# Performance work log

Measured on AMD Instinct MI355X. Metric: run time of the kernel, lower is better.

## Reference

```python
import jax, jax.numpy as jnp
import numpy as np

NHEADS = 16
SCALE_BASE = 512
GN_EPS = 1e-5


def rotate_every_two(x):
    x1 = x[..., ::2]
    x2 = x[..., 1::2]
    return jnp.stack((-x2, x1), axis=-1).reshape(x.shape)


def xpos_apply(x, downscale, offset=0):
    # x: [B, T, C]; XPOS over the FULL embedding dim (applied before head split)
    B, T, C = x.shape
    half = C // 2
    scale_vec = (jnp.arange(0, C, 2, dtype=jnp.float32) + 0.4 * C) / (1.4 * C)  # [half]
    min_pos = -(T + offset) // 2
    max_pos = T + offset + min_pos
    power = jnp.arange(min_pos, max_pos, dtype=jnp.float32) / SCALE_BASE  # [L]
    scale = scale_vec[None, :] ** power[:, None]  # [L, half]
    L = scale.shape[0]
    inv_freq = 1.0 / (10000.0 ** (jnp.arange(half, dtype=jnp.float32) / half))
    sinusoid = jnp.arange(L, dtype=jnp.float32)[:, None] * inv_freq[None, :]  # [L, half]
    sin, cos = jnp.sin(sinusoid), jnp.cos(sinusoid)
    if L > T:
        scale, sin, cos = scale[-T:], sin[-T:], cos[-T:]
    if downscale:
        scale = 1.0 / scale
    sin = jnp.repeat(sin * scale, 2, axis=-1)  # [T, C] (duplicate_interleave)
    cos = jnp.repeat(cos * scale, 2, axis=-1)
    return x * cos + rotate_every_two(x) * sin


def decay_mask(nheads, T):
    gamma = 1.0 - 2.0 ** (-5.0 - jnp.arange(nheads, dtype=jnp.float32))  # [H]
    idx = jnp.arange(T)
    diff = idx[:, None] - idx[None, :]  # [T, T]
    keep = diff >= 0
    m = gamma[:, None, None] ** jnp.where(keep, diff, 0).astype(jnp.float32)
    return jnp.where(keep[None, :, :], m, 0.0)  # [H, T, T]


def setup_inputs() -> dict:
    key = jax.random.key(0)
    ks = jax.random.split(key, 6)
    B, T, C = 2, 2048, 1024
    w_std = 0.02
    return {
        "x": jax.random.normal(ks[0], (B, T, C), jnp.float32),
        "w_qkvff": jax.random.normal(ks[1], (5 * C, C), jnp.float32) * w_std,
        "w_gated": jax.random.normal(ks[2], (C, C), jnp.float32) * w_std,
        "b_gated": jnp.zeros((C,), jnp.float32),
        "w_proj": jax.random.normal(ks[3], (C, C), jnp.float32) * w_std,
        "b_proj": jnp.zeros((C,), jnp.float32),
        "gn_w": jnp.ones((C,), jnp.float32),
        "gn_b": jnp.zeros((C,), jnp.float32),
        "w_ff": jax.random.normal(ks[4], (C, 2 * C), jnp.float32) * w_std,
        "rms_w": jnp.ones((C,), jnp.float32),
    }


def reference(x, w_qkvff, w_gated, b_gated, w_proj, b_proj, gn_w, gn_b, w_ff, rms_w):
    B, T, C = x.shape
    H = NHEADS
    hd = C // H
    # RMSNorm: x / clamp(||x|| * C^-0.5, 1e-8) * w
    nrm = jnp.sqrt(jnp.sum(x * x, axis=-1, keepdims=True)) * (C ** -0.5)
    x_ = x / jnp.maximum(nrm, 1e-8) * rms_w
    # fused qkvff projection (Linear, no bias): [B,T,5C]
    qkvff = jnp.einsum('btc,oc->bto', x_, w_qkvff)
    q, k, v, ff = jnp.split(qkvff, [C, 2 * C, 3 * C], axis=-1)
    q = xpos_apply(q, downscale=False)
    k = xpos_apply(k, downscale=True)
    # split heads -> [B,H,T,hd]
    q = q.reshape(B, T, H, hd).transpose(0, 2, 1, 3)
    k = k.reshape(B, T, H, hd).transpose(0, 2, 1, 3)
    v = v.reshape(B, T, H, hd).transpose(0, 2, 1, 3)
    # parallel retention: decay-masked QK^T @ V
    scores = jnp.einsum('bhtd,bhsd->bhts', q, k) * (hd ** -0.5)
    scores = scores * decay_mask(H, T)[None]
    y = jnp.einsum('bhts,bhsd->bhtd', scores, v)  # [B,H,T,hd]
    # GroupNorm(H groups) applied over flattened (B*T, C)
    yg = y.transpose(0, 2, 1, 3).reshape(B * T, H, hd)
    mu = jnp.mean(yg, axis=-1, keepdims=True)
    var = jnp.mean((yg - mu) ** 2, axis=-1, keepdims=True)
    yg = (yg - mu) / jnp.sqrt(var + GN_EPS)
    y = yg.reshape(B * T, C) * gn_w + gn_b
    y = y.reshape(B, T, C)
    # gated SiLU on raw x (pre-norm), then output proj
    y = jax.nn.silu(jnp.einsum('btc,oc->bto', x, w_gated) + b_gated) * y
    y = jnp.einsum('btc,oc->bto', y, w_proj) + b_proj
    # gated FFN branch: exact (erf) GELU then Linear(2C->C, no bias)
    ff_out = jnp.einsum('bte,ce->btc', jax.nn.gelu(ff, approximate=False), w_ff)
    return x + ff_out + y
```

## Files before the change

kernel.cpp:

```cpp
#include <hip/hip_runtime.h>
#include <math.h>

#define B_  2
#define T_  2048
#define C_  1024
#define H_  16
#define FC_ 5120

typedef __attribute__((ext_vector_type(8))) short  s16x8;
typedef __attribute__((ext_vector_type(4))) float  f32x4;
typedef __attribute__((ext_vector_type(2))) unsigned short u16x2;
typedef __attribute__((ext_vector_type(4))) unsigned short u16x4;
typedef __attribute__((ext_vector_type(8))) unsigned short u16x8;

__device__ __forceinline__ ushort f2bf(float f) {
    union { float f; unsigned u; } v; v.f = f;
    unsigned r = v.u + 0x7FFFu + ((v.u >> 16) & 1u);
    return (ushort)(r >> 16);
}
__device__ __forceinline__ float bf2f(ushort u) {
    union { unsigned u; float f; } v; v.u = (unsigned)u << 16; return v.f;
}

__global__ __launch_bounds__(256) void cvt_bf16_kernel(const float* __restrict__ src,
                                                       ushort* __restrict__ dst, int n8) {
    int i = blockIdx.x * 256 + threadIdx.x;
    if (i >= n8) return;
    float4 a = ((const float4*)src)[2*i];
    float4 b = ((const float4*)src)[2*i + 1];
    u16x8 o;
    o[0] = f2bf(a.x); o[1] = f2bf(a.y); o[2] = f2bf(a.z); o[3] = f2bf(a.w);
    o[4] = f2bf(b.x); o[5] = f2bf(b.y); o[6] = f2bf(b.z); o[7] = f2bf(b.w);
    *(u16x8*)(dst + 8*i) = o;
}

__global__ __launch_bounds__(256) void rmsnorm_kernel(const float* __restrict__ x,
                                                      const float* __restrict__ rms_w,
                                                      ushort* __restrict__ xn) {
    int row = blockIdx.x;
    int tid = threadIdx.x;
    float4 v = ((const float4*)(x + (size_t)row * C_))[tid];
    float ss = v.x*v.x + v.y*v.y + v.z*v.z + v.w*v.w;
    #pragma unroll
    for (int m = 32; m >= 1; m >>= 1) ss += __shfl_xor(ss, m);
    __shared__ float wsum[4];
    if ((tid & 63) == 0) wsum[tid >> 6] = ss;
    __syncthreads();
    float tot = wsum[0] + wsum[1] + wsum[2] + wsum[3];
    float nrm = sqrtf(tot) * 0.03125f;
    float inv = 1.0f / fmaxf(nrm, 1e-8f);
    float4 w = ((const float4*)rms_w)[tid];
    u16x4 o;
    o[0] = f2bf(v.x * inv * w.x);  o[1] = f2bf(v.y * inv * w.y);
    o[2] = f2bf(v.z * inv * w.z);  o[3] = f2bf(v.w * inv * w.w);
    *(u16x4*)(xn + (size_t)row * C_ + 4*tid) = o;
}

__global__ __launch_bounds__(256) void xpos_bf16_kernel(const ushort* __restrict__ qktmp,
                                                        ushort* __restrict__ qkv) {
    int bt = blockIdx.x;
    int t = bt & (T_ - 1);
    float tf = (float)t;
    const ushort* row = qktmp + (size_t)bt * 2048;
    ushort* orow = qkv + (size_t)bt * 3072;
    float power = (tf - 1024.0f) * (1.0f / 512.0f);
    for (int i = threadIdx.x; i < 512; i += 256) {
        float sv    = (2.0f * (float)i + 409.6f) * (1.0f / 1433.6f);
        float scale = exp2f(power * log2f(sv));
        float invf  = exp2f((float)i * (-13.287712379549449f / 512.0f));
        float ang   = tf * invf;
        float sn, cs;
        sincosf(ang, &sn, &cs);
        float rs = 1.0f / scale;
        int hh = i >> 5;
        float lg2g = log2f(1.0f - exp2f(-5.0f - (float)hh));
        float gq = exp2f(lg2g * tf) * 0.125f;
        float gk = exp2f(-lg2g * tf);
        u16x2 qi = *(const u16x2*)(row + 2*i);
        u16x2 ki = *(const u16x2*)(row + 1024 + 2*i);
        float qx = bf2f(qi[0]), qy = bf2f(qi[1]);
        float kx = bf2f(ki[0]), ky = bf2f(ki[1]);
        float qox = (qx*(cs*scale) - qy*(sn*scale)) * gq;
        float qoy = (qy*(cs*scale) + qx*(sn*scale)) * gq;
        float kox = (kx*(cs*rs) - ky*(sn*rs)) * gk;
        float koy = (ky*(cs*rs) + kx*(sn*rs)) * gk;
        u16x2 qo; qo[0] = f2bf(qox); qo[1] = f2bf(qoy);
        u16x2 ko; ko[0] = f2bf(kox); ko[1] = f2bf(koy);
        *(u16x2*)(orow + 2*i) = qo;
        *(u16x2*)(orow + 1024 + 2*i) = ko;
    }
}

template<int EPI, int BN>
__global__ __launch_bounds__(256) void gemm_bf16_kernel(
        const ushort* __restrict__ A, int lda,
        const ushort* __restrict__ W, int ldw,
        float* __restrict__ Cmat, int ldc, int K,
        const float* __restrict__ bias,
        const float* __restrict__ add1,
        const float* __restrict__ add2,
        ushort* __restrict__ oqk,
        ushort* __restrict__ ov,
        ushort* __restrict__ offb) {
    constexpr int NG = BN / 32;
    __shared__ __align__(16) ushort As[128*64];
    __shared__ __align__(16) ushort Bs[BN*64];
    int tid = threadIdx.x;
    int m0 = blockIdx.y * 128, n0 = blockIdx.x * BN;
    int wave = tid >> 6, lane = tid & 63;
    int lo = lane & 15, hi = lane >> 4;
    int wm = (wave >> 1) * 64, wn = (wave & 1) * (BN/2);
    int sra = tid >> 3, sua = tid & 7;
    f32x4 acc[4][NG] = {};

    u16x8 ra[4], rb[4];
    auto loadA = [&](int k0) {
        #pragma unroll
        for (int i = 0; i < 4; ++i)
            ra[i] = *(const u16x8*)(A + (size_t)(m0 + sra + 32*i) * lda + k0 + sua*8);
    };
    auto loadB = [&](int k0) {
        if constexpr (BN == 128) {
            #pragma unroll
            for (int i = 0; i < 4; ++i)
                rb[i] = *(const u16x8*)(W + (size_t)(n0 + sra + 32*i) * ldw + k0 + sua*8);
        } else {
            int r = tid >> 2, c = tid & 3;
            rb[0] = *(const u16x8*)(W + (size_t)(n0 + r) * ldw + k0 + c*8);
            rb[1] = *(const u16x8*)(W + (size_t)(n0 + r) * ldw + k0 + (c+4)*8);
        }
    };
    loadA(0); loadB(0);
    for (int k0 = 0;;) {
        __syncthreads();
        #pragma unroll
        for (int i = 0; i < 4; ++i) {
            int row = sra + 32*i;
            *(u16x8*)((char*)As + (row*128 + ((sua*16) ^ ((row & 7) << 4)))) = ra[i];
        }
        if constexpr (BN == 128) {
            #pragma unroll
            for (int i = 0; i < 4; ++i) {
                int row = sra + 32*i;
                *(u16x8*)((char*)Bs + (row*128 + ((sua*16) ^ ((row & 7) << 4)))) = rb[i];
            }
        } else {
            int r = tid >> 2, c = tid & 3, sw = (r & 7) << 4;
            *(u16x8*)((char*)Bs + (r*128 + ((c*16) ^ sw)))     = rb[0];
            *(u16x8*)((char*)Bs + (r*128 + (((c+4)*16) ^ sw))) = rb[1];
        }
        __syncthreads();
        k0 += 64;
        if (k0 < K) { loadA(k0); loadB(k0); }
        #pragma unroll
        for (int kc = 0; kc < 2; ++kc) {
            s16x8 af[4], bf[NG];
            #pragma unroll
            for (int g = 0; g < 4; ++g) {
                int arow = wm + g*16 + lo;
                af[g] = *(const s16x8*)((const char*)As +
                         arow*128 + ((kc*64 + hi*16) ^ ((arow & 7) << 4)));
            }
            #pragma unroll
            for (int g = 0; g < NG; ++g) {
                int brow = wn + g*16 + lo;
                bf[g] = *(const s16x8*)((const char*)Bs +
                         brow*128 + ((kc*64 + hi*16) ^ ((brow & 7) << 4)));
            }
            #pragma unroll
            for (int mg = 0; mg < 4; ++mg)
                #pragma unroll
                for (int ng = 0; ng < NG; ++ng)
                    acc[mg][ng] = __builtin_amdgcn_mfma_f32_16x16x32_bf16(
                        af[mg], bf[ng], acc[mg][ng], 0, 0, 0);
        }
        if (k0 >= K) break;
    }
    #pragma unroll
    for (int mg = 0; mg < 4; ++mg) {
        #pragma unroll
        for (int r = 0; r < 4; ++r) {
            size_t m = (size_t)(m0 + wm + mg*16 + hi*4 + r);
            #pragma unroll
            for (int ng = 0; ng < NG; ++ng) {
                int n = n0 + wn + ng*16 + lo;
                float v = acc[mg][ng][r];
                if constexpr (EPI == 3) {
                    if (n0 < 2048)      oqk[m*2048 + n] = f2bf(v);
                    else if (n0 < 3072) ov[m*3072 + n] = f2bf(v);
                    else offb[m*2048 + (n - 3072)] =
                             f2bf(0.5f * v * (1.0f + erff(v * 0.70710678118f)));
                } else {
                    if (EPI == 1) {
                        float s = v + bias[n];
                        v = s / (1.0f + expf(-s));
                    } else if (EPI == 2) {
                        v += bias[n] + add1[m*ldc + n] + add2[m*ldc + n];
                    }
                    Cmat[m*ldc + n] = v;
                }
            }
        }
    }
}

__global__ __launch_bounds__(256) void attn_mfma2_kernel(const ushort* __restrict__ qkv,
                                                         float* __restrict__ y) {
    __shared__ ushort Ks[2][64*64];
    __shared__ ushort Vt[2][64*64];
    __shared__ ushort Ss[4][16*64];
    int F = blockIdx.x;
    int o = (F & 7) * 64 + (F >> 3);
    int tta = o & 15;
    int h   = (o >> 4) & 15;
    int b   = o >> 8;
    int ttb = 31 - tta;
    int t0a = tta * 64, t0b = ttb * 64;
    int tid = threadIdx.x;
    int wave = tid >> 6, lane = tid & 63;
    int lo = lane & 15, hi = lane >> 4;
    const size_t bT = (size_t)b * T_;

    const ushort* qra = qkv + (bT + t0a + wave*16 + lo) * 3072 + h*64;
    const ushort* qrb = qkv + (bT + t0b + wave*16 + lo) * 3072 + h*64;
    s16x8 qa0 = *(const s16x8*)(qra + hi*8);
    s16x8 qa1 = *(const s16x8*)(qra + 32 + hi*8);
    s16x8 qb0 = *(const s16x8*)(qrb + hi*8);
    s16x8 qb1 = *(const s16x8*)(qrb + 32 + hi*8);
    f32x4 acca[4] = {}, accb[4] = {};

    int kr = tid >> 2, kc = tid & 3;
    int vd0 = (tid & 15) * 4, vs0 = (tid >> 4) * 4;
    u16x8 rka, rkb;
    u16x4 rv0, rv1, rv2, rv3;
    auto loadt = [&](int s0) {
        const ushort* src = qkv + (bT + s0 + kr) * 3072 + 1024 + h*64;
        rka = *(const u16x8*)(src + kc*8);
        rkb = *(const u16x8*)(src + (kc+4)*8);
        const ushort* vsrc = qkv + (bT + s0 + vs0) * 3072 + 2048 + h*64 + vd0;
        rv0 = *(const u16x4*)(vsrc);
        rv1 = *(const u16x4*)(vsrc + 3072);
        rv2 = *(const u16x4*)(vsrc + 2*3072);
        rv3 = *(const u16x4*)(vsrc + 3*3072);
    };
    int cur = 0;
    loadt(0);
    for (int st = 0; st <= ttb; ++st) {
        {
            int base = kr * 128, sw = (kr & 7) << 4;
            *(u16x8*)((char*)Ks[cur] + ((base + kc*16) ^ sw))     = rka;
            *(u16x8*)((char*)Ks[cur] + ((base + (kc+4)*16) ^ sw)) = rkb;
            #pragma unroll
            for (int i = 0; i < 4; ++i) {
                u16x4 o4; o4[0] = rv0[i]; o4[1] = rv1[i]; o4[2] = rv2[i]; o4[3] = rv3[i];
                int d = vd0 + i;
                *(u16x4*)((char*)Vt[cur] + ((d*128 + vs0*2) ^ ((d & 7) << 4))) = o4;
            }
        }
        __syncthreads();
        if (st < ttb) loadt((st + 1) * 64);

        auto compute = [&](s16x8 q0, s16x8 q1, f32x4* accy, bool diag) {
            f32x4 sacc[4] = {};
            #pragma unroll
            for (int sn = 0; sn < 4; ++sn) {
                int srow = sn*16 + lo;
                int rb2 = srow * 128, sw = (srow & 7) << 4;
                s16x8 kf0 = *(const s16x8*)((const char*)Ks[cur] + ((rb2 + hi*16) ^ sw));
                s16x8 kf1 = *(const s16x8*)((const char*)Ks[cur] + ((rb2 + 64 + hi*16) ^ sw));
                sacc[sn] = __builtin_amdgcn_mfma_f32_16x16x32_bf16(q0, kf0, sacc[sn], 0, 0, 0);
                sacc[sn] = __builtin_amdgcn_mfma_f32_16x16x32_bf16(q1, kf1, sacc[sn], 0, 0, 0);
            }
            #pragma unroll
            for (int sn = 0; sn < 4; ++sn) {
                int sl = sn*16 + lo;
                #pragma unroll
                for (int r = 0; r < 4; ++r) {
                    float v = sacc[sn][r];
                    if (diag && sl > wave*16 + hi*4 + r) v = 0.0f;
                    int tq = hi*4 + r;
                    *(ushort*)((char*)Ss[wave] + ((tq*128 + sl*2) ^ ((tq & 7) << 4))) = f2bf(v);
                }
            }
            s16x8 sa0 = *(const s16x8*)((const char*)Ss[wave] + ((lo*128 + hi*16) ^ ((lo & 7) << 4)));
            s16x8 sa1 = *(const s16x8*)((const char*)Ss[wave] + ((lo*128 + 64 + hi*16) ^ ((lo & 7) << 4)));
            #pragma unroll
            for (int dn = 0; dn < 4; ++dn) {
                int d = dn*16 + lo;
                int rb2 = d * 128, sw = (d & 7) << 4;
                s16x8 vf0 = *(const s16x8*)((const char*)Vt[cur] + ((rb2 + hi*16) ^ sw));
                s16x8 vf1 = *(const s16x8*)((const char*)Vt[cur] + ((rb2 + 64 + hi*16) ^ sw));
                accy[dn] = __builtin_amdgcn_mfma_f32_16x16x32_bf16(sa0, vf0, accy[dn], 0, 0, 0);
                accy[dn] = __builtin_amdgcn_mfma_f32_16x16x32_bf16(sa1, vf1, accy[dn], 0, 0, 0);
            }
        };
        compute(qb0, qb1, accb, st == ttb);
        if (st <= tta) compute(qa0, qa1, acca, st == tta);
        cur ^= 1;
    }
    #pragma unroll
    for (int dn = 0; dn < 4; ++dn) {
        #pragma unroll
        for (int r = 0; r < 4; ++r) {
            int ta = t0a + wave*16 + hi*4 + r;
            int tb = t0b + wave*16 + hi*4 + r;
            y[(bT + ta) * C_ + h*64 + dn*16 + lo] = acca[dn][r];
            y[(bT + tb) * C_ + h*64 + dn*16 + lo] = accb[dn][r];
        }
    }
}

__global__ __launch_bounds__(256) void gn_gate_kernel(const float* __restrict__ y,
                                                      const float* __restrict__ gate,
                                                      const float* __restrict__ gn_w,
                                                      const float* __restrict__ gn_b,
                                                      ushort* __restrict__ ygb) {
    int bt = blockIdx.x;
    int tid = threadIdx.x;
    float4 v = ((const float4*)(y + (size_t)bt * C_))[tid];
    float s1 = v.x + v.y + v.z + v.w;
    float s2 = v.x*v.x + v.y*v.y + v.z*v.z + v.w*v.w;
    #pragma unroll
    for (int m = 1; m < 16; m <<= 1) { s1 += __shfl_xor(s1, m); s2 += __shfl_xor(s2, m); }
    float mu   = s1 * (1.0f/64.0f);
    float var  = s2 * (1.0f/64.0f) - mu*mu;
    float rstd = rsqrtf(var + 1e-5f);
    float4 w  = ((const float4*)gn_w)[tid];
    float4 bb = ((const float4*)gn_b)[tid];
    float4 g  = ((const float4*)(gate + (size_t)bt * C_))[tid];
    u16x4 o;
    o[0] = f2bf(((v.x - mu)*rstd*w.x + bb.x) * g.x);
    o[1] = f2bf(((v.y - mu)*rstd*w.y + bb.y) * g.y);
    o[2] = f2bf(((v.z - mu)*rstd*w.z + bb.z) * g.z);
    o[3] = f2bf(((v.w - mu)*rstd*w.w + bb.w) * g.w);
    *(u16x4*)(ygb + (size_t)bt * C_ + 4*tid) = o;
}

extern "C" void kernel_launch(void* const* d_in, const int* in_sizes, int n_in,
                              void* d_out, int out_size, void* d_ws, size_t ws_size,
                              hipStream_t stream) {
    (void)in_sizes; (void)n_in; (void)out_size; (void)ws_size;
    const float* x       = (const float*)d_in[0];
    const float* w_qkvff = (const float*)d_in[1];
    const float* w_gated = (const float*)d_in[2];
    const float* b_gated = (const float*)d_in[3];
    const float* w_proj  = (const float*)d_in[4];
    const float* b_proj  = (const float*)d_in[5];
    const float* gn_w    = (const float*)d_in[6];
    const float* gn_b    = (const float*)d_in[7];
    const float* w_ff    = (const float*)d_in[8];
    const float* rms_w   = (const float*)d_in[9];
    float* out = (float*)d_out;

    const size_t NTOK = (size_t)B_ * T_;
    float* buf0   = (float*)d_ws;
    float* buf1   = buf0 + NTOK * C_;
    float* buf2   = buf1 + NTOK * C_;
    ushort* qkvb  = (ushort*)(buf2 + NTOK * C_);
    ushort* qktmp = qkvb + NTOK * 3072;
    ushort* xb    = qktmp + NTOK * 2048;
    ushort* xnb   = xb + NTOK * C_;
    ushort* ffb   = xnb + NTOK * C_;
    ushort* ygb   = ffb + NTOK * 2048;
    ushort* wqb   = ygb + NTOK * C_;
    ushort* wgb   = wqb + (size_t)FC_ * C_;
    ushort* wpb   = wgb + (size_t)C_ * C_;
    ushort* wfb   = wpb + (size_t)C_ * C_;

    cvt_bf16_kernel<<<2048, 256, 0, stream>>>(x, xb, 524288);
    cvt_bf16_kernel<<<2560, 256, 0, stream>>>(w_qkvff, wqb, 655360);
    cvt_bf16_kernel<<<512,  256, 0, stream>>>(w_gated, wgb, 131072);
    cvt_bf16_kernel<<<512,  256, 0, stream>>>(w_proj,  wpb, 131072);
    cvt_bf16_kernel<<<1024, 256, 0, stream>>>(w_ff,    wfb, 262144);
    rmsnorm_kernel<<<4096, 256, 0, stream>>>(x, rms_w, xnb);
    gemm_bf16_kernel<3,128><<<dim3(40, 32), 256, 0, stream>>>(
        xnb, C_, wqb, C_, nullptr, 0, C_, nullptr, nullptr, nullptr, qktmp, qkvb, ffb);
    xpos_bf16_kernel<<<4096, 256, 0, stream>>>(qktmp, qkvb);
    attn_mfma2_kernel<<<512, 256, 0, stream>>>(qkvb, buf1);
    gemm_bf16_kernel<1,64><<<dim3(16, 32), 256, 0, stream>>>(
        xb, C_, wgb, C_, buf2, C_, C_, b_gated, nullptr, nullptr, nullptr, nullptr, nullptr);
    gn_gate_kernel<<<4096, 256, 0, stream>>>(buf1, buf2, gn_w, gn_b, ygb);
    gemm_bf16_kernel<0,64><<<dim3(16, 32), 256, 0, stream>>>(
        ffb, 2*C_, wfb, 2*C_, buf0, C_, 2*C_, nullptr, nullptr, nullptr, nullptr, nullptr, nullptr);
    gemm_bf16_kernel<2,64><<<dim3(16, 32), 256, 0, stream>>>(
        ygb, C_, wpb, C_, out, C_, C_, b_proj, x, buf0, nullptr, nullptr, nullptr);
}
```

Baseline: 324.4 us.

## Use direct global-to-LDS loads in GEMM and merge bf16 conversion launches

The GEMM tile loads now use global_load_lds to copy A and B tiles straight into shared memory. The XOR swizzle moves into the global column index, so the register staging and software prefetch of the next tile are gone. The five fp32-to-bf16 conversion launches are also merged into one kernel that picks its source by block index. In exchange, the GEMM loses its overlap of the next tile's loads with the current MFMA work, since loads are now issued after the barrier with no double buffering.

```diff
diff --git a/kernel.cpp b/kernel.cpp
--- a/kernel.cpp
+++ b/kernel.cpp
@@ -13,6 +13,9 @@
 typedef __attribute__((ext_vector_type(4))) unsigned short u16x4;
 typedef __attribute__((ext_vector_type(8))) unsigned short u16x8;
 
+#define AS1 __attribute__((address_space(1)))
+#define AS3 __attribute__((address_space(3)))
+
 __device__ __forceinline__ ushort f2bf(float f) {
     union { float f; unsigned u; } v; v.f = f;
     unsigned r = v.u + 0x7FFFu + ((v.u >> 16) & 1u);
@@ -21,17 +24,30 @@
 __device__ __forceinline__ float bf2f(ushort u) {
     union { unsigned u; float f; } v; v.u = (unsigned)u << 16; return v.f;
 }
-
-__global__ __launch_bounds__(256) void cvt_bf16_kernel(const float* __restrict__ src,
-                                                       ushort* __restrict__ dst, int n8) {
+__device__ __forceinline__ void gload16(const void* g, void* l) {
+    __builtin_amdgcn_global_load_lds((const AS1 unsigned int*)g,
+                                     (AS3 unsigned int*)l, 16, 0, 0);
+}
+
+__global__ __launch_bounds__(256) void cvt_all_kernel(
+        const float* __restrict__ x, const float* __restrict__ wq,
+        const float* __restrict__ wg, const float* __restrict__ wp,
+        const float* __restrict__ wf,
+        ushort* __restrict__ xb, ushort* __restrict__ wqb, ushort* __restrict__ wgb,
+        ushort* __restrict__ wpb, ushort* __restrict__ wfb) {
     int i = blockIdx.x * 256 + threadIdx.x;
-    if (i >= n8) return;
-    float4 a = ((const float4*)src)[2*i];
-    float4 b = ((const float4*)src)[2*i + 1];
+    const float* src; ushort* dst; int off;
+    if (i < 524288)       { src = x;  dst = xb;  off = i; }
+    else if (i < 1179648) { src = wq; dst = wqb; off = i - 524288; }
+    else if (i < 1310720) { src = wg; dst = wgb; off = i - 1179648; }
+    else if (i < 1441792) { src = wp; dst = wpb; off = i - 1310720; }
+    else                  { src = wf; dst = wfb; off = i - 1441792; }
+    float4 a = ((const float4*)src)[2*off];
+    float4 b = ((const float4*)src)[2*off + 1];
     u16x8 o;
     o[0] = f2bf(a.x); o[1] = f2bf(a.y); o[2] = f2bf(a.z); o[3] = f2bf(a.w);
     o[4] = f2bf(b.x); o[5] = f2bf(b.y); o[6] = f2bf(b.z); o[7] = f2bf(b.w);
-    *(u16x8*)(dst + 8*i) = o;
+    *(u16x8*)(dst + 8*off) = o;
 }
 
 __global__ __launch_bounds__(256) void rmsnorm_kernel(const float* __restrict__ x,
@@ -110,48 +126,34 @@
     int wave = tid >> 6, lane = tid & 63;
     int lo = lane & 15, hi = lane >> 4;
     int wm = (wave >> 1) * 64, wn = (wave & 1) * (BN/2);
-    int sra = tid >> 3, sua = tid & 7;
+    int lrow  = lane >> 3;
+    int gcol  = ((lane & 7) ^ lrow) * 8;
     f32x4 acc[4][NG] = {};
 
-    u16x8 ra[4], rb[4];
-    auto loadA = [&](int k0) {
-        #pragma unroll
-        for (int i = 0; i < 4; ++i)
-            ra[i] = *(const u16x8*)(A + (size_t)(m0 + sra + 32*i) * lda + k0 + sua*8);
-    };
-    auto loadB = [&](int k0) {
-        if constexpr (BN == 128) {
-            #pragma unroll
-            for (int i = 0; i < 4; ++i)
-                rb[i] = *(const u16x8*)(W + (size_t)(n0 + sra + 32*i) * ldw + k0 + sua*8);
-        } else {
-            int r = tid >> 2, c = tid & 3;
-            rb[0] = *(const u16x8*)(W + (size_t)(n0 + r) * ldw + k0 + c*8);
-            rb[1] = *(const u16x8*)(W + (size_t)(n0 + r) * ldw + k0 + (c+4)*8);
-        }
-    };
-    loadA(0); loadB(0);
-    for (int k0 = 0;;) {
+    for (int k0 = 0; k0 < K; k0 += 64) {
         __syncthreads();
         #pragma unroll
         for (int i = 0; i < 4; ++i) {
-            int row = sra + 32*i;
-            *(u16x8*)((char*)As + (row*128 + ((sua*16) ^ ((row & 7) << 4)))) = ra[i];
+            int c = wave*4 + i;
+            gload16(A + (size_t)(m0 + c*8 + lrow) * lda + k0 + gcol,
+                    (ushort*)As + c*512);
         }
         if constexpr (BN == 128) {
             #pragma unroll
             for (int i = 0; i < 4; ++i) {
-                int row = sra + 32*i;
-                *(u16x8*)((char*)Bs + (row*128 + ((sua*16) ^ ((row & 7) << 4)))) = rb[i];
+                int c = wave*4 + i;
+                gload16(W + (size_t)(n0 + c*8 + lrow) * ldw + k0 + gcol,
+                        (ushort*)Bs + c*512);
             }
         } else {
-            int r = tid >> 2, c = tid & 3, sw = (r & 7) << 4;
-            *(u16x8*)((char*)Bs + (r*128 + ((c*16) ^ sw)))     = rb[0];
-            *(u16x8*)((char*)Bs + (r*128 + (((c+4)*16) ^ sw))) = rb[1];
+            #pragma unroll
+            for (int i = 0; i < 2; ++i) {
+                int c = wave*2 + i;
+                gload16(W + (size_t)(n0 + c*8 + lrow) * ldw + k0 + gcol,
+                        (ushort*)Bs + c*512);
+            }
         }
         __syncthreads();
-        k0 += 64;
-        if (k0 < K) { loadA(k0); loadB(k0); }
         #pragma unroll
         for (int kc = 0; kc < 2; ++kc) {
             s16x8 af[4], bf[NG];
@@ -174,7 +176,6 @@
                     acc[mg][ng] = __builtin_amdgcn_mfma_f32_16x16x32_bf16(
                         af[mg], bf[ng], acc[mg][ng], 0, 0, 0);
         }
-        if (k0 >= K) break;
     }
     #pragma unroll
     for (int mg = 0; mg < 4; ++mg) {
@@ -367,11 +368,8 @@
     ushort* wpb   = wgb + (size_t)C_ * C_;
     ushort* wfb   = wpb + (size_t)C_ * C_;
 
-    cvt_bf16_kernel<<<2048, 256, 0, stream>>>(x, xb, 524288);
-    cvt_bf16_kernel<<<2560, 256, 0, stream>>>(w_qkvff, wqb, 655360);
-    cvt_bf16_kernel<<<512,  256, 0, stream>>>(w_gated, wgb, 131072);
-    cvt_bf16_kernel<<<512,  256, 0, stream>>>(w_proj,  wpb, 131072);
-    cvt_bf16_kernel<<<1024, 256, 0, stream>>>(w_ff,    wfb, 262144);
+    cvt_all_kernel<<<6656, 256, 0, stream>>>(x, w_qkvff, w_gated, w_proj, w_ff,
+                                             xb, wqb, wgb, wpb, wfb);
     rmsnorm_kernel<<<4096, 256, 0, stream>>>(x, rms_w, xnb);
     gemm_bf16_kernel<3,128><<<dim3(40, 32), 256, 0, stream>>>(
         xnb, C_, wqb, C_, nullptr, 0, C_, nullptr, nullptr, nullptr, qktmp, qkvb, ffb);
```

Result: no change. 328.5 us (+1.3%).
